# Kernel optimization log

Hardware: AMD Instinct MI355X
Metric: run time of the kernel (lower is better)

## Reference

```python
import jax, jax.numpy as jnp
import numpy as np
import math

B, T, D, K, KER, H = 2, 2048, 1024, 16, 7, 2048


def _decay_logit_init(k: int, dmin: float = 0.9, dmax: float = 0.999) -> np.ndarray:
    decays = np.exp(np.linspace(math.log(dmin), math.log(dmax), k))
    return (np.log(decays) - np.log1p(-decays)).astype(np.float32)


def setup_inputs() -> dict:
    key = jax.random.key(0)
    ks = jax.random.split(key, 12)
    s = 0.02
    return {
        "x": jax.random.normal(ks[0], (B, T, D), jnp.float32),
        "conv_w": jax.random.normal(ks[1], (D, KER), jnp.float32) * s,   # depthwise causal conv taps
        "gate_w": jax.random.normal(ks[2], (D, D), jnp.float32) * (D ** -0.5),
        "gate_b": jnp.zeros((D,), jnp.float32),
        "up_w": jax.random.normal(ks[3], (D, H), jnp.float32) * (D ** -0.5),
        "up_b": jnp.zeros((H,), jnp.float32),
        "down_w": jax.random.normal(ks[4], (H, D), jnp.float32) * (H ** -0.5),
        "down_b": jnp.zeros((D,), jnp.float32),
        "sin_w": jax.random.normal(ks[5], (D, K * D), jnp.float32) * (D ** -0.5),
        "sout_w": jax.random.normal(ks[6], (K * D, D), jnp.float32) * ((K * D) ** -0.5),
        "decay_logit": jnp.asarray(_decay_logit_init(K)),
        "gl_w": jax.random.normal(ks[7], (D, 1), jnp.float32) * (D ** -0.5),
        "gl_b": jnp.zeros((1,), jnp.float32),
    }


def _rmsnorm(x, eps=1e-6):
    return x * jax.lax.rsqrt(jnp.mean(x * x, axis=-1, keepdims=True) + eps)


def reference(x, conv_w, gate_w, gate_b, up_w, up_b, down_w, down_b,
              sin_w, sout_w, decay_logit, gl_w, gl_b):
    b, t, d = x.shape
    k_taps = conv_w.shape[1]
    nk = decay_logit.shape[0]

    u = _rmsnorm(x)  # (B,T,D)

    # --- local mixer: causal depthwise conv (zero history buffer) + sigmoid gate + SiLU MLP ---
    u_pad = jnp.pad(u, ((0, 0), (k_taps - 1, 0), (0, 0)))
    y = sum(conv_w[:, j] * u_pad[:, j:j + t, :] for j in range(k_taps))  # (B,T,D)
    g = jax.nn.sigmoid(u @ gate_w + gate_b)
    h = y * g
    local = jax.nn.silu(h @ up_w + up_b) @ down_w + down_b

    # --- state bank: K leaky integrators, s_t = a*s_{t-1} + (1-a)*z_t ---
    z = (u @ sin_w).reshape(b, t, nk, d)  # (B,T,K,D)
    a = jax.nn.sigmoid(decay_logit)[:, None]  # (K,1)

    def step(s, z_t):
        s = a * s + (1.0 - a) * z_t
        return s, s

    s0 = jnp.zeros((b, nk, d), x.dtype)
    _, S = jax.lax.scan(step, s0, jnp.swapaxes(z, 0, 1))  # (T,B,K,D)
    S = jnp.swapaxes(S, 0, 1).reshape(b, t, nk * d)
    long_path = S @ sout_w  # (B,T,D)

    # --- gate fusion + residual (memory table is empty at init -> mem term == 0) ---
    g_long = jax.nn.sigmoid(u @ gl_w + gl_b)  # (B,T,1)
    return x + local + g_long * long_path
```

## Files before the change

### kernel.cpp

```cpp
#include <hip/hip_runtime.h>
#include <cstdint>
#include <cstddef>

typedef __attribute__((ext_vector_type(8))) short short8;
typedef __attribute__((ext_vector_type(4))) float floatx4;

#define DEV static __device__ __forceinline__

#define PSTRIDE ((size_t)4096 * 1024)

DEV unsigned short f2bf(float f) {
  union { float f; uint32_t u; } v; v.f = f;
  uint32_t r = v.u + 0x7fffu + ((v.u >> 16) & 1u);
  return (unsigned short)(r >> 16);
}
DEV float bf2f(unsigned short h) {
  union { uint32_t u; float f; } v; v.u = ((uint32_t)h) << 16; return v.f;
}
DEV float sigmoidf_(float x) { return 1.f / (1.f + __expf(-x)); }

DEV void gld_lds16(const unsigned short* g, unsigned short* l) {
  __builtin_amdgcn_global_load_lds(
      (const __attribute__((address_space(1))) void*)g,
      (__attribute__((address_space(3))) void*)l, 16, 0, 0);
}

__global__ __launch_bounds__(256) void transpose_kernel(
    const float* __restrict__ W, unsigned short* __restrict__ Wt,
    int Kdim, int Ndim) {
  __shared__ float tile[32][33];
  const int n0 = blockIdx.x * 32;
  const int k0 = blockIdx.y * 32;
  const int tx = threadIdx.x & 31;
  const int ty = threadIdx.x >> 5;
#pragma unroll
  for (int r = 0; r < 32; r += 8)
    tile[ty + r][tx] = W[(size_t)(k0 + ty + r) * Ndim + n0 + tx];
  __syncthreads();
#pragma unroll
  for (int r = 0; r < 32; r += 8)
    Wt[(size_t)(n0 + ty + r) * Kdim + k0 + tx] = f2bf(tile[tx][ty + r]);
}

__global__ __launch_bounds__(256) void cast_kernel(
    const float* __restrict__ W, unsigned short* __restrict__ Wb) {
  const size_t i = (size_t)blockIdx.x * 256 + threadIdx.x;
  const float4 v = ((const float4*)W)[i];
  ushort4 o;
  o.x = f2bf(v.x); o.y = f2bf(v.y); o.z = f2bf(v.z); o.w = f2bf(v.w);
  ((ushort4*)Wb)[i] = o;
}

__global__ __launch_bounds__(256) void rmsnorm_kernel(
    const float* __restrict__ x, const float* __restrict__ gl_w,
    const float* __restrict__ gl_b, unsigned short* __restrict__ u,
    float* __restrict__ gl_logit) {
  const int row = blockIdx.x;
  const int tid = threadIdx.x;
  const float4 v = ((const float4*)(x + (size_t)row * 1024))[tid];
  float ss = v.x * v.x + v.y * v.y + v.z * v.z + v.w * v.w;
#pragma unroll
  for (int o = 32; o > 0; o >>= 1) ss += __shfl_down(ss, o, 64);
  __shared__ float red[4];
  if ((tid & 63) == 0) red[tid >> 6] = ss;
  __syncthreads();
  const float tot = red[0] + red[1] + red[2] + red[3];
  const float r = rsqrtf(tot * (1.f / 1024.f) + 1e-6f);
  const float ux = v.x * r, uy = v.y * r, uz = v.z * r, uw = v.w * r;
  ushort4 ub;
  ub.x = f2bf(ux); ub.y = f2bf(uy); ub.z = f2bf(uz); ub.w = f2bf(uw);
  ((ushort4*)(u + (size_t)row * 1024))[tid] = ub;
  const float4 w4 = ((const float4*)gl_w)[tid];
  float dot = ux * w4.x + uy * w4.y + uz * w4.z + uw * w4.w;
#pragma unroll
  for (int o = 32; o > 0; o >>= 1) dot += __shfl_down(dot, o, 64);
  __syncthreads();
  if ((tid & 63) == 0) red[tid >> 6] = dot;
  __syncthreads();
  if (tid == 0) gl_logit[row] = red[0] + red[1] + red[2] + red[3] + gl_b[0];
}

template <int EPI>
__global__ __launch_bounds__(256, 2) void gemm_bt(
    const unsigned short* __restrict__ A, const unsigned short* __restrict__ Bt,
    const float* __restrict__ bias, void* __restrict__ Cout, int Ndim, int Kdim) {
  __shared__ unsigned short As[128 * 32];
  __shared__ unsigned short Bs[128 * 32];
  const int tid = threadIdx.x;
  const int wave = tid >> 6;
  const int lane = tid & 63;
  const size_t row0 = (size_t)blockIdx.x * 128;
  const size_t col0 = (size_t)blockIdx.y * 128;

  const int srow = wave * 32 + (lane >> 2);
  const int kofs = (lane & 3) * 8;
  const unsigned short* pA0 = A + (row0 + srow) * (size_t)Kdim + kofs;
  const unsigned short* pA1 = A + (row0 + srow + 16) * (size_t)Kdim + kofs;
  const unsigned short* pB0 = Bt + (col0 + srow) * (size_t)Kdim + kofs;
  const unsigned short* pB1 = Bt + (col0 + srow + 16) * (size_t)Kdim + kofs;
  unsigned short* lA0 = &As[(wave * 2 + 0) * 512];
  unsigned short* lA1 = &As[(wave * 2 + 1) * 512];
  unsigned short* lB0 = &Bs[(wave * 2 + 0) * 512];
  unsigned short* lB1 = &Bs[(wave * 2 + 1) * 512];

  const int wm = (wave & 1) * 64;
  const int wn = (wave >> 1) * 64;
  const int lr = lane & 15;
  const int lq = lane >> 4;
  const int a_off = (wm + lr) * 32 + lq * 8;
  const int b_off = (wn + lr) * 32 + lq * 8;

  floatx4 acc[4][4];
#pragma unroll
  for (int i = 0; i < 4; i++)
#pragma unroll
    for (int j = 0; j < 4; j++) acc[i][j] = floatx4{0.f, 0.f, 0.f, 0.f};

  for (int kt = 0; kt < Kdim; kt += 32) {
    __syncthreads();
    gld_lds16(pA0, lA0);
    gld_lds16(pA1, lA1);
    gld_lds16(pB0, lB0);
    gld_lds16(pB1, lB1);
    pA0 += 32; pA1 += 32; pB0 += 32; pB1 += 32;
    __syncthreads();
    short8 af[4], bfr[4];
#pragma unroll
    for (int i = 0; i < 4; i++) af[i] = *(const short8*)&As[a_off + i * 16 * 32];
#pragma unroll
    for (int j = 0; j < 4; j++) bfr[j] = *(const short8*)&Bs[b_off + j * 16 * 32];
#pragma unroll
    for (int i = 0; i < 4; i++)
#pragma unroll
      for (int j = 0; j < 4; j++)
        acc[i][j] = __builtin_amdgcn_mfma_f32_16x16x32_bf16(af[i], bfr[j], acc[i][j], 0, 0, 0);
  }

#pragma unroll
  for (int i = 0; i < 4; i++) {
    const size_t rbase = row0 + wm + 16 * i + lq * 4;
#pragma unroll
    for (int j = 0; j < 4; j++) {
      const size_t c = col0 + wn + 16 * j + lr;
#pragma unroll
      for (int r = 0; r < 4; r++) {
        float v = acc[i][j][r];
        const size_t off = (rbase + r) * (size_t)Ndim + c;
        if constexpr (EPI == 2) {
          v += bias[c];
          ((unsigned short*)Cout)[off] = f2bf(v * sigmoidf_(v));
        } else {
          ((unsigned short*)Cout)[off] = f2bf(v);
        }
      }
    }
  }
}

__global__ __launch_bounds__(256, 2) void gemm_gate(
    const unsigned short* __restrict__ A, const unsigned short* __restrict__ Bt,
    const float* __restrict__ gate_b, const float* __restrict__ conv_w,
    unsigned short* __restrict__ h) {
  __shared__ unsigned short As[128 * 32];
  __shared__ unsigned short Bs[128 * 32];
  const int tid = threadIdx.x;
  const int wave = tid >> 6;
  const int lane = tid & 63;
  const size_t row0 = (size_t)blockIdx.x * 128;
  const size_t col0 = (size_t)blockIdx.y * 128;
  const int Kdim = 1024;

  const int srow = wave * 32 + (lane >> 2);
  const int kofs = (lane & 3) * 8;
  const unsigned short* pA0 = A + (row0 + srow) * (size_t)Kdim + kofs;
  const unsigned short* pA1 = A + (row0 + srow + 16) * (size_t)Kdim + kofs;
  const unsigned short* pB0 = Bt + (col0 + srow) * (size_t)Kdim + kofs;
  const unsigned short* pB1 = Bt + (col0 + srow + 16) * (size_t)Kdim + kofs;
  unsigned short* lA0 = &As[(wave * 2 + 0) * 512];
  unsigned short* lA1 = &As[(wave * 2 + 1) * 512];
  unsigned short* lB0 = &Bs[(wave * 2 + 0) * 512];
  unsigned short* lB1 = &Bs[(wave * 2 + 1) * 512];

  const int wm = (wave & 1) * 64;
  const int wn = (wave >> 1) * 64;
  const int lr = lane & 15;
  const int lq = lane >> 4;
  const int a_off = (wm + lr) * 32 + lq * 8;
  const int b_off = (wn + lr) * 32 + lq * 8;

  floatx4 acc[4][4];
#pragma unroll
  for (int i = 0; i < 4; i++)
#pragma unroll
    for (int j = 0; j < 4; j++) acc[i][j] = floatx4{0.f, 0.f, 0.f, 0.f};

  for (int kt = 0; kt < Kdim; kt += 32) {
    __syncthreads();
    gld_lds16(pA0, lA0);
    gld_lds16(pA1, lA1);
    gld_lds16(pB0, lB0);
    gld_lds16(pB1, lB1);
    pA0 += 32; pA1 += 32; pB0 += 32; pB1 += 32;
    __syncthreads();
    short8 af[4], bfr[4];
#pragma unroll
    for (int i = 0; i < 4; i++) af[i] = *(const short8*)&As[a_off + i * 16 * 32];
#pragma unroll
    for (int j = 0; j < 4; j++) bfr[j] = *(const short8*)&Bs[b_off + j * 16 * 32];
#pragma unroll
    for (int i = 0; i < 4; i++)
#pragma unroll
      for (int j = 0; j < 4; j++)
        acc[i][j] = __builtin_amdgcn_mfma_f32_16x16x32_bf16(af[i], bfr[j], acc[i][j], 0, 0, 0);
  }

#pragma unroll
  for (int i = 0; i < 4; i++) {
    const size_t rbase = row0 + wm + 16 * i + lq * 4;
#pragma unroll
    for (int j = 0; j < 4; j++) {
      const size_t c = col0 + wn + 16 * j + lr;
      const float gb = gate_b[c];
      float cw[7];
#pragma unroll
      for (int jj = 0; jj < 7; ++jj) cw[jj] = conv_w[c * 7 + jj];
#pragma unroll
      for (int r = 0; r < 4; r++) {
        const size_t row = rbase + r;
        const int t = (int)(row & 2047);
        const unsigned short* up = A + row * 1024 + c;
        float conv = 0.f;
#pragma unroll
        for (int jj = 0; jj < 7; ++jj) {
          const int tt = t - 6 + jj;
          if (tt >= 0) conv += cw[jj] * bf2f(up[(jj - 6) * 1024]);
        }
        const float logit = acc[i][j][r] + gb;
        h[row * 1024 + c] = f2bf(conv * sigmoidf_(logit));
      }
    }
  }
}

template <int MODE>
__global__ __launch_bounds__(512, 2) void gemm256(
    const unsigned short* __restrict__ A, const unsigned short* __restrict__ B,
    unsigned short* __restrict__ Cbase, int splitLen) {
  __shared__ unsigned short lds[65536];
  constexpr int LD = (MODE == 2) ? 2048 : 16384;
  const int tid = threadIdx.x;
  const int w = tid >> 6;
  const int l = tid & 63;
  const int wr = w >> 2;
  const int wc = w & 3;
  const size_t row0 = (size_t)blockIdx.x * 256;
  const size_t col0 = (size_t)blockIdx.y * 256;
  const int z = blockIdx.z;
  int k0, nkt;
  if constexpr (MODE == 0) {
    k0 = z * splitLen;
    int klen = 16384 - k0; if (klen > splitLen) klen = splitLen;
    nkt = klen >> 6;
  } else if constexpr (MODE == 1) {
    k0 = z << 10; nkt = 16;
  } else {
    k0 = z << 9; nkt = 8;
  }

  const int lrow = l >> 3;
  const int lcol = (l & 7) ^ lrow;
  const unsigned short* gA = A + (row0 + w * 16 + lrow) * (size_t)LD + k0 + lcol * 8;
  const unsigned short* gB = B + (col0 + w * 16 + lrow) * (size_t)LD + k0 + lcol * 8;
  const int sA = w * 1024;
  const int sB = 16384 + w * 1024;

  const int lr = l & 15;
  const int lq = l >> 4;
  const int aoff = (wr * 128 + lr) * 64 + ((lq ^ (lr & 7)) * 8);
  const int boff = 16384 + (wc * 64 + lr) * 64 + ((lq ^ (lr & 7)) * 8);

#define STG_A(bufb, st, h) { \
    const unsigned short* s_ = gA + (size_t)(h) * (128 * LD) + (size_t)(st) * 64; \
    unsigned short* d_ = &lds[(bufb) * 32768 + (h) * 8192 + sA]; \
    gld_lds16(s_, d_); gld_lds16(s_ + 8 * LD, d_ + 512); }
#define STG_B(bufb, st, h) { \
    const unsigned short* s_ = gB + (size_t)(h) * (128 * LD) + (size_t)(st) * 64; \
    unsigned short* d_ = &lds[(bufb) * 32768 + (h) * 8192 + sB]; \
    gld_lds16(s_, d_); gld_lds16(s_ + 8 * LD, d_ + 512); }

  floatx4 acc[8][4];
#pragma unroll
  for (int i = 0; i < 8; ++i)
#pragma unroll
    for (int j = 0; j < 4; ++j) acc[i][j] = floatx4{0.f, 0.f, 0.f, 0.f};

  STG_A(0, 0, 0) STG_A(0, 0, 1) STG_B(0, 0, 0) STG_B(0, 0, 1)
  STG_B(1, 1, 0) STG_B(1, 1, 1)
  asm volatile("s_waitcnt vmcnt(4)" ::: "memory");
  __builtin_amdgcn_s_barrier();

  short8 bfr[4][2];

#define MM1(IP, AR, NJ, KK) \
  acc[AR][NJ] = __builtin_amdgcn_mfma_f32_16x16x32_bf16(af_[IP][KK], bfr[NJ][KK], acc[AR][NJ], 0, 0, 0);

#define PHASE(Q, STAGE_STMT, TAIL) { \
    short8 af_[2][2]; \
    af_[0][0] = *(const short8*)&lds[cb + aoff + (Q * 2 + 0) * 1024]; \
    af_[0][1] = *(const short8*)&lds[cb + (aoff ^ 32) + (Q * 2 + 0) * 1024]; \
    af_[1][0] = *(const short8*)&lds[cb + aoff + (Q * 2 + 1) * 1024]; \
    af_[1][1] = *(const short8*)&lds[cb + (aoff ^ 32) + (Q * 2 + 1) * 1024]; \
    STAGE_STMT \
    __builtin_amdgcn_s_barrier(); \
    asm volatile("s_waitcnt lgkmcnt(0)" ::: "memory"); \
    __builtin_amdgcn_sched_barrier(0); \
    __builtin_amdgcn_s_setprio(1); \
    MM1(0, Q * 2 + 0, 0, 0) MM1(1, Q * 2 + 1, 0, 0) \
    MM1(0, Q * 2 + 0, 1, 0) MM1(1, Q * 2 + 1, 1, 0) \
    MM1(0, Q * 2 + 0, 2, 0) MM1(1, Q * 2 + 1, 2, 0) \
    MM1(0, Q * 2 + 0, 3, 0) MM1(1, Q * 2 + 1, 3, 0) \
    MM1(0, Q * 2 + 0, 0, 1) MM1(1, Q * 2 + 1, 0, 1) \
    MM1(0, Q * 2 + 0, 1, 1) MM1(1, Q * 2 + 1, 1, 1) \
    MM1(0, Q * 2 + 0, 2, 1) MM1(1, Q * 2 + 1, 2, 1) \
    MM1(0, Q * 2 + 0, 3, 1) MM1(1, Q * 2 + 1, 3, 1) \
    __builtin_amdgcn_s_setprio(0); \
    TAIL; \
    __builtin_amdgcn_s_barrier(); }

  for (int S = 0; S < nkt; ++S) {
    const int cur = S & 1;
    const int oth = cur ^ 1;
    const int cb = cur * 32768;
    const int t1 = (S + 1 < nkt) ? S + 1 : nkt - 1;
    const int t2 = (S + 2 < nkt) ? S + 2 : nkt - 1;
#pragma unroll
    for (int nj = 0; nj < 4; ++nj) {
      bfr[nj][0] = *(const short8*)&lds[cb + boff + nj * 1024];
      bfr[nj][1] = *(const short8*)&lds[cb + (boff ^ 32) + nj * 1024];
    }
    PHASE(0, STG_A(oth, t1, 0), )
    PHASE(1, STG_A(oth, t1, 1), )
    PHASE(2, STG_B(cur, t2, 0), )
    PHASE(3, STG_B(cur, t2, 1), asm volatile("s_waitcnt vmcnt(4)" ::: "memory"))
  }

#pragma unroll
  for (int mi = 0; mi < 8; ++mi) {
    const size_t r0 = row0 + wr * 128 + mi * 16 + lq * 4;
#pragma unroll
    for (int nj = 0; nj < 4; ++nj) {
      const size_t c = col0 + wc * 64 + nj * 16 + lr;
#pragma unroll
      for (int r = 0; r < 4; ++r) {
        const float v = acc[mi][nj][r];
        if constexpr (MODE == 1)
          Cbase[(r0 + r) * 16384 + ((size_t)z << 10) + c] = f2bf(v);
        else
          Cbase[(size_t)z * PSTRIDE + (r0 + r) * 1024 + c] = f2bf(v);
      }
    }
  }
#undef PHASE
#undef MM1
#undef STG_A
#undef STG_B
}

__global__ __launch_bounds__(256) void fold4_kernel(
    const float* __restrict__ x, const unsigned short* __restrict__ dp,
    const float* __restrict__ down_b, float* __restrict__ out) {
  const size_t idx = (size_t)blockIdx.x * 256 + threadIdx.x;
  const float s = bf2f(dp[idx]) + bf2f(dp[idx + PSTRIDE]) +
                  bf2f(dp[idx + 2 * PSTRIDE]) + bf2f(dp[idx + 3 * PSTRIDE]);
  out[idx] = x[idx] + s + down_b[idx & 1023];
}

template <int NS>
__global__ __launch_bounds__(256) void reduceNg_kernel(
    const unsigned short* __restrict__ p, const float* __restrict__ gl,
    float* __restrict__ out) {
  const size_t idx = (size_t)blockIdx.x * 256 + threadIdx.x;
  const float g = sigmoidf_(gl[idx >> 10]);
  float s = 0.f;
#pragma unroll
  for (int i = 0; i < NS; ++i) s += bf2f(p[idx + (size_t)i * PSTRIDE]);
  out[idx] += g * s;
}

__global__ __launch_bounds__(256) void scan1u_kernel(
    const unsigned short* __restrict__ u, const float* __restrict__ decay_logit,
    float* __restrict__ carry) {
  const int gid = blockIdx.x * 256 + threadIdx.x;
  const int d = gid & 1023;
  const int b = (gid >> 10) & 1;
  const int c = gid >> 11;
  float a[16], s[16];
#pragma unroll
  for (int k = 0; k < 16; ++k) { a[k] = sigmoidf_(decay_logit[k]); s[k] = 0.f; }
  const unsigned short* p = u + ((size_t)b * 2048 + c * 128) * 1024 + d;
#pragma unroll 2
  for (int t = 0; t < 128; ++t) {
    const float uv = bf2f(*p);
    p += 1024;
#pragma unroll
    for (int k = 0; k < 16; ++k) s[k] = fmaf(a[k], s[k], (1.f - a[k]) * uv);
  }
#pragma unroll
  for (int k = 0; k < 16; ++k)
    carry[(size_t)((c * 2 + b) * 16 + k) * 1024 + d] = s[k];
}

__global__ __launch_bounds__(256) void scan2u_kernel(
    float* __restrict__ carry, const float* __restrict__ decay_logit) {
  const int gid = blockIdx.x * 256 + threadIdx.x;
  const int d = gid & 1023;
  const int k = (gid >> 10) & 15;
  const int b = gid >> 14;
  const float a = sigmoidf_(decay_logit[k]);
  float aL = a;
#pragma unroll
  for (int i = 0; i < 7; ++i) aL *= aL;
  float s = 0.f;
#pragma unroll
  for (int c = 0; c < 16; ++c) {
    const size_t idx = (size_t)((c * 2 + b) * 16 + k) * 1024 + d;
    const float Lc = carry[idx];
    carry[idx] = s;
    s = fmaf(aL, s, Lc);
  }
}

__global__ __launch_bounds__(256) void scan3u_kernel(
    const unsigned short* __restrict__ u, const float* __restrict__ decay_logit,
    const float* __restrict__ carry, unsigned short* __restrict__ Ucat) {
  const int gid = blockIdx.x * 256 + threadIdx.x;
  const int d = gid & 1023;
  const int k = (gid >> 10) & 15;
  const int b = (gid >> 14) & 1;
  const int c = gid >> 15;
  const float a = sigmoidf_(decay_logit[k]);
  const float na = 1.f - a;
  float s = carry[(size_t)((c * 2 + b) * 16 + k) * 1024 + d];
  const unsigned short* p = u + ((size_t)b * 2048 + c * 128) * 1024 + d;
  unsigned short* q = Ucat + ((size_t)b * 2048 + c * 128) * 16384 + k * 1024 + d;
#pragma unroll 4
  for (int t = 0; t < 128; ++t) {
    s = fmaf(a, s, na * bf2f(*p));
    *q = f2bf(s);
    p += 1024;
    q += 16384;
  }
}

extern "C" void kernel_launch(void* const* d_in, const int* in_sizes, int n_in,
                              void* d_out, int out_size, void* d_ws,
                              size_t ws_size, hipStream_t stream) {
  const float* x      = (const float*)d_in[0];
  const float* conv_w = (const float*)d_in[1];
  const float* gate_w = (const float*)d_in[2];
  const float* gate_b = (const float*)d_in[3];
  const float* up_w   = (const float*)d_in[4];
  const float* up_b   = (const float*)d_in[5];
  const float* down_w = (const float*)d_in[6];
  const float* down_b = (const float*)d_in[7];
  const float* sin_w  = (const float*)d_in[8];
  const float* sout_w = (const float*)d_in[9];
  const float* decay  = (const float*)d_in[10];
  const float* gl_w   = (const float*)d_in[11];
  const float* gl_b   = (const float*)d_in[12];
  float* out = (float*)d_out;
  char* ws = (char*)d_ws;

  const bool big = ws_size >= (((size_t)192 << 20) + ((size_t)1 << 16));

  auto Ucat = (unsigned short*)(ws + ((size_t)0 << 20));
  auto GWT  = (unsigned short*)(ws + ((size_t)0 << 20));
  auto Hb   = (unsigned short*)(ws + ((size_t)18 << 20));
  auto UWT  = (unsigned short*)(ws + ((size_t)26 << 20));
  auto Mb   = (unsigned short*)(ws + ((size_t)30 << 20));
  auto DWT  = (unsigned short*)(ws + ((size_t)46 << 20));
  auto DP   = (unsigned short*)(ws + ((size_t)50 << 20));
  auto SB   = (unsigned short*)(ws + ((size_t)0 << 20));
  auto OT   = (unsigned short*)(ws + ((size_t)32 << 20));
  auto MT   = (unsigned short*)(ws + ((size_t)128 << 20));
  auto U    = (unsigned short*)(ws + ((size_t)160 << 20));
  auto P    = (unsigned short*)(ws + ((size_t)160 << 20));
  auto CARRY= (float*)(ws + ((size_t)168 << 20));
  auto GL   = (float*)(ws + (big ? ((size_t)192 << 20) : ((size_t)184 << 20)));

  rmsnorm_kernel<<<4096, 256, 0, stream>>>(x, gl_w, gl_b, U, GL);

  transpose_kernel<<<dim3(32, 32), 256, 0, stream>>>(gate_w, GWT, 1024, 1024);
  gemm_gate<<<dim3(32, 8), 256, 0, stream>>>(U, GWT, gate_b, conv_w, Hb);
  transpose_kernel<<<dim3(64, 32), 256, 0, stream>>>(up_w, UWT, 1024, 2048);
  gemm_bt<2><<<dim3(32, 16), 256, 0, stream>>>(Hb, UWT, up_b, Mb, 2048, 1024);
  transpose_kernel<<<dim3(32, 64), 256, 0, stream>>>(down_w, DWT, 2048, 1024);
  gemm256<2><<<dim3(16, 4, 4), 512, 0, stream>>>(Mb, DWT, DP, 512);
  fold4_kernel<<<16384, 256, 0, stream>>>(x, DP, down_b, out);

  cast_kernel<<<16384, 256, 0, stream>>>(sin_w, SB);
  transpose_kernel<<<dim3(32, 512), 256, 0, stream>>>(sout_w, OT, 16384, 1024);
  gemm256<1><<<dim3(4, 4, 16), 512, 0, stream>>>(OT, SB, MT, 1024);

  scan1u_kernel<<<128, 256, 0, stream>>>(U, decay, CARRY);
  scan2u_kernel<<<128, 256, 0, stream>>>(CARRY, decay);
  scan3u_kernel<<<2048, 256, 0, stream>>>(U, decay, CARRY, Ucat);

  if (big) {
    gemm256<0><<<dim3(16, 4, 4), 512, 0, stream>>>(Ucat, MT, P, 4096);
    reduceNg_kernel<4><<<16384, 256, 0, stream>>>(P, GL, out);
  } else {
    gemm256<0><<<dim3(16, 4, 3), 512, 0, stream>>>(Ucat, MT, P, 5504);
    reduceNg_kernel<3><<<16384, 256, 0, stream>>>(P, GL, out);
  }
}
```

Baseline: 532.7 us.

## Software-pipeline LDS fragment loads with double-buffered A registers in GEMM loop

Restructures the GEMM main loop so A-fragment LDS reads for the next phase are issued before the current phase's MFMAs, using two register buffers (afA/afB). B fragments for the next k-tile are prefetched during the last phase's MFMAs. Each phase previously waited on lgkmcnt(0) before its MFMAs; this overlaps LDS latency with compute and drops one barrier per phase. The cost is higher VGPR pressure and a subtler vmcnt/barrier ordering that has to stay correct for the buffer reuse.

After: 542.1 us. No clear change (+1.8%).

```diff
diff --git a/kernel.cpp b/kernel.cpp
--- a/kernel.cpp
+++ b/kernel.cpp
@@ -298,50 +298,86 @@
   STG_B(1, 1, 0) STG_B(1, 1, 1)
   asm volatile("s_waitcnt vmcnt(4)" ::: "memory");
   __builtin_amdgcn_s_barrier();
+  __builtin_amdgcn_sched_barrier(0);
 
   short8 bfr[4][2];
-
-#define MM1(IP, AR, NJ, KK) \
-  acc[AR][NJ] = __builtin_amdgcn_mfma_f32_16x16x32_bf16(af_[IP][KK], bfr[NJ][KK], acc[AR][NJ], 0, 0, 0);
-
-#define PHASE(Q, STAGE_STMT, TAIL) { \
-    short8 af_[2][2]; \
-    af_[0][0] = *(const short8*)&lds[cb + aoff + (Q * 2 + 0) * 1024]; \
-    af_[0][1] = *(const short8*)&lds[cb + (aoff ^ 32) + (Q * 2 + 0) * 1024]; \
-    af_[1][0] = *(const short8*)&lds[cb + aoff + (Q * 2 + 1) * 1024]; \
-    af_[1][1] = *(const short8*)&lds[cb + (aoff ^ 32) + (Q * 2 + 1) * 1024]; \
-    STAGE_STMT \
-    __builtin_amdgcn_s_barrier(); \
-    asm volatile("s_waitcnt lgkmcnt(0)" ::: "memory"); \
-    __builtin_amdgcn_sched_barrier(0); \
-    __builtin_amdgcn_s_setprio(1); \
-    MM1(0, Q * 2 + 0, 0, 0) MM1(1, Q * 2 + 1, 0, 0) \
-    MM1(0, Q * 2 + 0, 1, 0) MM1(1, Q * 2 + 1, 1, 0) \
-    MM1(0, Q * 2 + 0, 2, 0) MM1(1, Q * 2 + 1, 2, 0) \
-    MM1(0, Q * 2 + 0, 3, 0) MM1(1, Q * 2 + 1, 3, 0) \
-    MM1(0, Q * 2 + 0, 0, 1) MM1(1, Q * 2 + 1, 0, 1) \
-    MM1(0, Q * 2 + 0, 1, 1) MM1(1, Q * 2 + 1, 1, 1) \
-    MM1(0, Q * 2 + 0, 2, 1) MM1(1, Q * 2 + 1, 2, 1) \
-    MM1(0, Q * 2 + 0, 3, 1) MM1(1, Q * 2 + 1, 3, 1) \
-    __builtin_amdgcn_s_setprio(0); \
-    TAIL; \
-    __builtin_amdgcn_s_barrier(); }
+  short8 afA[2][2], afB[2][2];
+
+#define LD_AF(DST, CB, MI) \
+    DST[0][0] = *(const short8*)&lds[(CB) + aoff + (MI) * 1024]; \
+    DST[0][1] = *(const short8*)&lds[(CB) + (aoff ^ 32) + (MI) * 1024]; \
+    DST[1][0] = *(const short8*)&lds[(CB) + aoff + ((MI) + 1) * 1024]; \
+    DST[1][1] = *(const short8*)&lds[(CB) + (aoff ^ 32) + ((MI) + 1) * 1024];
+
+#define LD_BF(CB, NJ) \
+    bfr[NJ][0] = *(const short8*)&lds[(CB) + boff + (NJ) * 1024]; \
+    bfr[NJ][1] = *(const short8*)&lds[(CB) + (boff ^ 32) + (NJ) * 1024];
+
+#define MM1(AF, IP, AR, NJ, KK) \
+  acc[AR][NJ] = __builtin_amdgcn_mfma_f32_16x16x32_bf16(AF[IP][KK], bfr[NJ][KK], acc[AR][NJ], 0, 0, 0);
+
+#define MFMA16(AF, R0) \
+  MM1(AF, 0, R0, 0, 0) MM1(AF, 1, (R0) + 1, 0, 0) \
+  MM1(AF, 0, R0, 1, 0) MM1(AF, 1, (R0) + 1, 1, 0) \
+  MM1(AF, 0, R0, 2, 0) MM1(AF, 1, (R0) + 1, 2, 0) \
+  MM1(AF, 0, R0, 3, 0) MM1(AF, 1, (R0) + 1, 3, 0) \
+  MM1(AF, 0, R0, 0, 1) MM1(AF, 1, (R0) + 1, 0, 1) \
+  MM1(AF, 0, R0, 1, 1) MM1(AF, 1, (R0) + 1, 1, 1) \
+  MM1(AF, 0, R0, 2, 1) MM1(AF, 1, (R0) + 1, 2, 1) \
+  MM1(AF, 0, R0, 3, 1) MM1(AF, 1, (R0) + 1, 3, 1)
+
+#define MFMA8(AF, R0, N0) \
+  MM1(AF, 0, R0, N0, 0) MM1(AF, 1, (R0) + 1, N0, 0) \
+  MM1(AF, 0, R0, (N0) + 1, 0) MM1(AF, 1, (R0) + 1, (N0) + 1, 0) \
+  MM1(AF, 0, R0, N0, 1) MM1(AF, 1, (R0) + 1, N0, 1) \
+  MM1(AF, 0, R0, (N0) + 1, 1) MM1(AF, 1, (R0) + 1, (N0) + 1, 1)
+
+#define PH_END \
+  __builtin_amdgcn_sched_barrier(0); \
+  __builtin_amdgcn_s_barrier(); \
+  __builtin_amdgcn_sched_barrier(0);
+
+  LD_AF(afA, 0, 0)
+  LD_BF(0, 0) LD_BF(0, 1) LD_BF(0, 2) LD_BF(0, 3)
 
   for (int S = 0; S < nkt; ++S) {
     const int cur = S & 1;
     const int oth = cur ^ 1;
     const int cb = cur * 32768;
+    const int ob = oth * 32768;
     const int t1 = (S + 1 < nkt) ? S + 1 : nkt - 1;
     const int t2 = (S + 2 < nkt) ? S + 2 : nkt - 1;
-#pragma unroll
-    for (int nj = 0; nj < 4; ++nj) {
-      bfr[nj][0] = *(const short8*)&lds[cb + boff + nj * 1024];
-      bfr[nj][1] = *(const short8*)&lds[cb + (boff ^ 32) + nj * 1024];
-    }
-    PHASE(0, STG_A(oth, t1, 0), )
-    PHASE(1, STG_A(oth, t1, 1), )
-    PHASE(2, STG_B(cur, t2, 0), )
-    PHASE(3, STG_B(cur, t2, 1), asm volatile("s_waitcnt vmcnt(4)" ::: "memory"))
+
+    STG_A(oth, t1, 0)
+    LD_AF(afB, cb, 2)
+    __builtin_amdgcn_s_setprio(1);
+    MFMA16(afA, 0)
+    __builtin_amdgcn_s_setprio(0);
+    PH_END
+    STG_A(oth, t1, 1)
+    LD_AF(afA, cb, 4)
+    __builtin_amdgcn_s_setprio(1);
+    MFMA16(afB, 2)
+    __builtin_amdgcn_s_setprio(0);
+    PH_END
+    STG_B(cur, t2, 0)
+    LD_AF(afB, cb, 6)
+    __builtin_amdgcn_s_setprio(1);
+    MFMA16(afA, 4)
+    __builtin_amdgcn_s_setprio(0);
+    PH_END
+    STG_B(cur, t2, 1)
+    asm volatile("s_waitcnt vmcnt(2)" ::: "memory");
+    __builtin_amdgcn_s_barrier();
+    __builtin_amdgcn_sched_barrier(0);
+    LD_AF(afA, ob, 0)
+    __builtin_amdgcn_s_setprio(1);
+    MFMA8(afB, 6, 0)
+    LD_BF(ob, 0) LD_BF(ob, 1)
+    MFMA8(afB, 6, 2)
+    LD_BF(ob, 2) LD_BF(ob, 3)
+    __builtin_amdgcn_s_setprio(0);
+    PH_END
   }
 
 #pragma unroll
@@ -360,8 +396,12 @@
       }
     }
   }
-#undef PHASE
+#undef PH_END
+#undef MFMA8
+#undef MFMA16
 #undef MM1
+#undef LD_BF
+#undef LD_AF
 #undef STG_A
 #undef STG_B
 }
```
